# Optimization experiments

Measured on AMD Instinct MI355X. Metric: run time of the kernel, lower is better.

Reference implementation:

```python
import jax, jax.numpy as jnp
import numpy as np

EPS = 1e-5
K = 20

def knn_idx(x, k):
    # x: (B, C, N); returns indices of k nearest neighbors (incl. self), (B, N, k)
    xx = jnp.sum(x * x, axis=1, keepdims=True)            # (B,1,N)
    inner = -2.0 * jnp.einsum('bcn,bcm->bnm', x, x)       # (B,N,N)
    d = -jnp.swapaxes(xx, 1, 2) - inner - xx              # -||xi - xj||^2
    return jax.lax.top_k(d, k)[1]

def graph_feature(x, k):
    # x: (B, C, N) -> (B, 2C, N, k) with [neighbor - center, center]
    B, C, N = x.shape
    idx = knn_idx(x, k)                                   # (B,N,k)
    feat = jnp.swapaxes(x, 1, 2)                          # (B,N,C)
    nb = jax.vmap(lambda f, i: f[i])(feat, idx)           # (B,N,k,C) gather
    ctr = jnp.broadcast_to(feat[:, :, None, :], nb.shape)
    out = jnp.concatenate([nb - ctr, ctr], axis=-1)       # (B,N,k,2C)
    return jnp.transpose(out, (0, 3, 1, 2))

def bn(x, g, b, m, v):
    # inference-mode batchnorm over channel axis 1
    shape = (1, -1) + (1,) * (x.ndim - 2)
    inv = g / jnp.sqrt(v + EPS)
    return x * inv.reshape(shape) + (b - m * inv).reshape(shape)

def edge_block(x, W, g, b, m, v):
    f = graph_feature(x, K)                               # (B,2C,N,k)
    h = jnp.einsum('bcnk,oc->bonk', f, W)                 # 1x1 conv, no bias
    h = jax.nn.relu(bn(h, g, b, m, v))
    return jnp.max(h, axis=-1)                            # max over k -> (B,O,N)

def _forward(x, W1, W2, W3, W4, W5,
             g1, b1, m1, v1, g2, b2, m2, v2, g3, b3, m3, v3,
             g4, b4, m4, v4, g5, b5, m5, v5, g6, b6, m6, v6,
             g7, b7, m7, v7, L1W, L2W, L2b, L3W, L3b):
    x1 = edge_block(x, W1, g1, b1, m1, v1)                # (B,64,N)
    x2 = edge_block(x1, W2, g2, b2, m2, v2)               # (B,64,N)
    x3 = edge_block(x2, W3, g3, b3, m3, v3)               # (B,128,N)
    x4 = edge_block(x3, W4, g4, b4, m4, v4)               # (B,256,N)
    cat = jnp.concatenate([x1, x2, x3, x4], axis=1)       # (B,512,N)
    h = jnp.einsum('bcn,oc->bon', cat, W5)                # conv5 1x1
    h = jax.nn.relu(bn(h, g5, b5, m5, v5))
    h = jnp.max(h, axis=-1)                               # adaptive max pool -> (B,1024)
    h = jax.nn.relu(bn(h @ L1W.T, g6, b6, m6, v6))        # dropout = identity (eval)
    h = jax.nn.relu(bn(h @ L2W.T + L2b, g7, b7, m7, v7))
    return h @ L3W.T + L3b                                # (B, num_classes)

def _bn_params(keys, c):
    k0, k1, k2, k3 = keys
    g = jax.random.uniform(k0, (c,), jnp.float32, 0.5, 1.5)
    b = 0.1 * jax.random.normal(k1, (c,), jnp.float32)
    m = 0.1 * jax.random.normal(k2, (c,), jnp.float32)
    v = jax.random.uniform(k3, (c,), jnp.float32, 0.5, 1.5)
    return g, b, m, v

def setup_inputs() -> dict:
    key = jax.random.key(0)
    ks = jax.random.split(key, 40)
    d = {}
    d['x'] = jax.random.normal(ks[0], (8, 4, 1024), jnp.float32)
    def w(k, o, i):
        return jax.random.normal(k, (o, i), jnp.float32) * np.float32(np.sqrt(2.0 / i))
    d['W1'] = w(ks[1], 64, 8)
    d['W2'] = w(ks[2], 64, 128)
    d['W3'] = w(ks[3], 128, 128)
    d['W4'] = w(ks[4], 256, 256)
    d['W5'] = w(ks[5], 1024, 512)
    for i, c in enumerate([64, 64, 128, 256, 1024, 512, 256]):
        g, b, m, v = _bn_params(jax.random.split(ks[6 + i], 4), c)
        d[f'g{i+1}'], d[f'b{i+1}'], d[f'm{i+1}'], d[f'v{i+1}'] = g, b, m, v
    d['L1W'] = w(ks[20], 512, 1024)
    d['L2W'] = w(ks[21], 256, 512)
    d['L2b'] = 0.1 * jax.random.normal(ks[22], (256,), jnp.float32)
    d['L3W'] = w(ks[23], 8, 256)
    d['L3b'] = 0.1 * jax.random.normal(ks[24], (8,), jnp.float32)
    return d

def reference(x, W1, W2, W3, W4, W5,
              g1, b1, m1, v1, g2, b2, m2, v2, g3, b3, m3, v3,
              g4, b4, m4, v4, g5, b5, m5, v5, g6, b6, m6, v6,
              g7, b7, m7, v7, L1W, L2W, L2b, L3W, L3b):
    return _forward(x, W1, W2, W3, W4, W5,
                    g1, b1, m1, v1, g2, b2, m2, v2, g3, b3, m3, v3,
                    g4, b4, m4, v4, g5, b5, m5, v5, g6, b6, m6, v6,
                    g7, b7, m7, v7, L1W, L2W, L2b, L3W, L3b)
```

## Files before the change

### kernel.cpp

```cpp
#include <hip/hip_runtime.h>
#include <cstdint>

#define BB 8
#define NN 1024
#define KK 20
#define EPSV 1e-5f

typedef __attribute__((ext_vector_type(8))) short bf16x8;
typedef __attribute__((ext_vector_type(4))) float f32x4;

__device__ __forceinline__ unsigned fenc(float f) {
  unsigned u = __float_as_uint(f);
  return (u & 0x80000000u) ? ~u : (u | 0x80000000u);
}
__device__ __forceinline__ float fdec(unsigned u) {
  u = (u & 0x80000000u) ? (u & 0x7FFFFFFFu) : ~u;
  return __uint_as_float(u);
}
__device__ __forceinline__ unsigned short f2bf(float f) {
  unsigned u = __float_as_uint(f);
  unsigned r = u + 0x7FFFu + ((u >> 16) & 1u);
  return (unsigned short)(r >> 16);
}
__device__ __forceinline__ unsigned mbcnt64(unsigned long long m) {
  unsigned r = __builtin_amdgcn_mbcnt_lo((unsigned)m, 0u);
  return __builtin_amdgcn_mbcnt_hi((unsigned)(m >> 32), r);
}

template<int C>
__global__ __launch_bounds__(256) void xx_kernel(const float* __restrict__ x, float* __restrict__ xx) {
  int p = blockIdx.x * 256 + threadIdx.x;
  if (p >= BB * NN) return;
  int b = p >> 10, n = p & (NN - 1);
  const float* xb = x + (size_t)b * C * NN + n;
  float s = 0.f;
  #pragma unroll
  for (int c = 0; c < C; ++c) { float t = xb[(size_t)c * NN]; s = fmaf(t, t, s); }
  xx[p] = s;
}

template<int C>
__global__ __launch_bounds__(256) void dist_kernel(const float* __restrict__ x, const float* __restrict__ xx,
                                                   float* __restrict__ d, int b0) {
  constexpr int CC = (C < 32) ? C : 32;
  __shared__ __align__(16) float xi[CC][64];
  __shared__ __align__(16) float xj[CC][64];
  int bl = blockIdx.z, b = b0 + bl;
  int i0 = blockIdx.y * 64, j0 = blockIdx.x * 64;
  int t = threadIdx.x;
  int tj = t & 15, ti = t >> 4;
  float acc[4][4] = {};
  const float* xb = x + (size_t)b * C * NN;
  for (int c0 = 0; c0 < C; c0 += CC) {
    __syncthreads();
    for (int p = t; p < CC * 16; p += 256) {
      int cc = p >> 4, col = (p & 15) * 4;
      *reinterpret_cast<float4*>(&xi[cc][col]) =
        *reinterpret_cast<const float4*>(&xb[(size_t)(c0 + cc) * NN + i0 + col]);
      *reinterpret_cast<float4*>(&xj[cc][col]) =
        *reinterpret_cast<const float4*>(&xb[(size_t)(c0 + cc) * NN + j0 + col]);
    }
    __syncthreads();
    #pragma unroll
    for (int cc = 0; cc < CC; ++cc) {
      float4 A  = *reinterpret_cast<const float4*>(&xi[cc][ti * 4]);
      float4 Bv = *reinterpret_cast<const float4*>(&xj[cc][tj * 4]);
      float av[4] = {A.x, A.y, A.z, A.w};
      float bv[4] = {Bv.x, Bv.y, Bv.z, Bv.w};
      #pragma unroll
      for (int a = 0; a < 4; ++a)
        #pragma unroll
        for (int q = 0; q < 4; ++q)
          acc[a][q] = fmaf(av[a], bv[q], acc[a][q]);
    }
  }
  #pragma unroll
  for (int a = 0; a < 4; ++a) {
    int i = i0 + ti * 4 + a;
    float xxi = xx[b * NN + i];
    float4 o;
    o.x = 2.f * acc[a][0] - xxi - xx[b * NN + j0 + tj * 4 + 0];
    o.y = 2.f * acc[a][1] - xxi - xx[b * NN + j0 + tj * 4 + 1];
    o.z = 2.f * acc[a][2] - xxi - xx[b * NN + j0 + tj * 4 + 2];
    o.w = 2.f * acc[a][3] - xxi - xx[b * NN + j0 + tj * 4 + 3];
    *reinterpret_cast<float4*>(&d[((size_t)bl * NN + i) * NN + j0 + tj * 4]) = o;
  }
}

__global__ __launch_bounds__(256) void topk_kernel(const float* __restrict__ d, int* __restrict__ idx, int b0) {
  int t = threadIdx.x;
  int wave = t >> 6, lane = t & 63;
  int bl = blockIdx.y, b = b0 + bl;
  int i = blockIdx.x * 4 + wave;
  const float* row = d + ((size_t)bl * NN + i) * NN;

  unsigned v[16];
  #pragma unroll
  for (int p = 0; p < 4; ++p) {
    float4 f = *reinterpret_cast<const float4*>(&row[p * 256 + lane * 4]);
    v[p * 4 + 0] = fenc(f.x);
    v[p * 4 + 1] = fenc(f.y);
    v[p * 4 + 2] = fenc(f.z);
    v[p * 4 + 3] = fenc(f.w);
  }

  unsigned long long lo = 0, hi = 0xFFFFFFFFull;
  while (lo < hi) {
    unsigned long long mid = lo + ((hi - lo + 1) >> 1);
    unsigned mt = (unsigned)mid;
    int c = 0;
    #pragma unroll
    for (int e = 0; e < 16; ++e)
      c += __popcll(__ballot(v[e] >= mt));
    if (c >= KK) lo = mid; else hi = mid - 1;
  }
  unsigned T = (unsigned)lo;

  int* op = idx + ((size_t)b * NN + i) * KK;
  int base = 0, n1 = 0;
  #pragma unroll
  for (int e = 0; e < 16; ++e) {
    unsigned long long mask = __ballot(v[e] > T);
    unsigned mb = mbcnt64(mask);
    if (v[e] > T) op[base + mb] = (e >> 2) * 256 + lane * 4 + (e & 3);
    base += __popcll(mask);
  }
  n1 = base;
  int need = KK - n1;
  int neq = 0;
  #pragma unroll
  for (int e = 0; e < 16; ++e) neq += __popcll(__ballot(v[e] == T));
  if (neq == need) {
    #pragma unroll
    for (int e = 0; e < 16; ++e) {
      unsigned long long mask = __ballot(v[e] == T);
      unsigned mb = mbcnt64(mask);
      if (v[e] == T) op[base + mb] = (e >> 2) * 256 + lane * 4 + (e & 3);
      base += __popcll(mask);
    }
  } else {
    unsigned taken = 0;
    for (int s = 0; s < need; ++s) {
      int jm = 1 << 30;
      #pragma unroll
      for (int e = 0; e < 16; ++e) {
        if (v[e] == T && !((taken >> e) & 1u)) {
          int j = (e >> 2) * 256 + lane * 4 + (e & 3);
          jm = jm < j ? jm : j;
        }
      }
      #pragma unroll
      for (int st = 1; st < 64; st <<= 1) {
        int oj = __shfl_xor(jm, st);
        jm = jm < oj ? jm : oj;
      }
      if (lane == ((jm >> 2) & 63)) {
        int e = (((jm >> 8) << 2) | (jm & 3));
        taken |= 1u << e;
        op[base + s] = jm;
      }
    }
  }
}

template<int C, int O>
__global__ __launch_bounds__(256) void pgemm_kernel(const float* __restrict__ x, const float* __restrict__ W,
                                                    float* __restrict__ Plo, float* __restrict__ Phi) {
  constexpr int CC = (C < 64) ? C : 64;
  __shared__ __align__(16) float xs[CC][64];
  __shared__ __align__(16) float wls[CC][68];
  __shared__ __align__(16) float whs[CC][68];
  int b = blockIdx.z;
  int o0 = blockIdx.y * 64, n0 = blockIdx.x * 64;
  int t = threadIdx.x;
  int tn = t & 15, to = t >> 4;
  float accl[4][4] = {}, acch[4][4] = {};
  const float* xb = x + (size_t)b * C * NN;
  for (int c0 = 0; c0 < C; c0 += CC) {
    __syncthreads();
    for (int p = t; p < CC * 64; p += 256) {
      int cc = p >> 6, col = p & 63;
      xs[cc][col] = xb[(size_t)(c0 + cc) * NN + n0 + col];
    }
    for (int p = t; p < 64 * CC; p += 256) {
      int ol = p / CC, cc = p % CC;
      wls[cc][ol] = W[(size_t)(o0 + ol) * (2 * C) + c0 + cc];
      whs[cc][ol] = W[(size_t)(o0 + ol) * (2 * C) + C + c0 + cc];
    }
    __syncthreads();
    #pragma unroll
    for (int cc = 0; cc < CC; ++cc) {
      float4 X  = *reinterpret_cast<const float4*>(&xs[cc][tn * 4]);
      float4 Wl = *reinterpret_cast<const float4*>(&wls[cc][to * 4]);
      float4 Wh = *reinterpret_cast<const float4*>(&whs[cc][to * 4]);
      float xv[4] = {X.x, X.y, X.z, X.w};
      float wl[4] = {Wl.x, Wl.y, Wl.z, Wl.w};
      float wh[4] = {Wh.x, Wh.y, Wh.z, Wh.w};
      #pragma unroll
      for (int a = 0; a < 4; ++a)
        #pragma unroll
        for (int q = 0; q < 4; ++q) {
          accl[a][q] = fmaf(wl[a], xv[q], accl[a][q]);
          acch[a][q] = fmaf(wh[a], xv[q], acch[a][q]);
        }
    }
  }
  #pragma unroll
  for (int a = 0; a < 4; ++a) {
    int o = o0 + to * 4 + a;
    size_t base = ((size_t)b * O + o) * NN + n0 + tn * 4;
    float4 vl = {accl[a][0], accl[a][1], accl[a][2], accl[a][3]};
    float4 vh = {acch[a][0], acch[a][1], acch[a][2], acch[a][3]};
    *reinterpret_cast<float4*>(&Plo[base]) = vl;
    *reinterpret_cast<float4*>(&Phi[base]) = vh;
  }
}

__global__ __launch_bounds__(256) void edgemax_kernel(const float* __restrict__ Plo, const float* __restrict__ Phi,
    const int* __restrict__ idx, const float* __restrict__ g, const float* __restrict__ bt,
    const float* __restrict__ m, const float* __restrict__ v,
    float* __restrict__ xout, int O) {
  __shared__ __align__(16) float srow[4][NN];
  __shared__ __align__(16) float sphi[4][64];
  __shared__ int   sidx[64 * KK];
  __shared__ float sinv[32], ssb[32];
  int b = blockIdx.z, n0 = blockIdx.y * 64, o0 = blockIdx.x * 32;
  int t = threadIdx.x;
  if (t < 32) {
    float inv = g[o0 + t] / sqrtf(v[o0 + t] + EPSV);
    sinv[t] = inv; ssb[t] = bt[o0 + t] - m[o0 + t] * inv;
  }
  for (int p = t; p < 64 * KK; p += 256) sidx[p] = idx[((size_t)b * NN + n0) * KK + p];
  const float* plobase = Plo + (size_t)b * O * NN;
  const float* phibase = Phi + (size_t)b * O * NN;
  float4 cur0 = *reinterpret_cast<const float4*>(&plobase[(size_t)(o0 + 0) * NN + t * 4]);
  float4 cur1 = *reinterpret_cast<const float4*>(&plobase[(size_t)(o0 + 1) * NN + t * 4]);
  float4 cur2 = *reinterpret_cast<const float4*>(&plobase[(size_t)(o0 + 2) * NN + t * 4]);
  float4 cur3 = *reinterpret_cast<const float4*>(&plobase[(size_t)(o0 + 3) * NN + t * 4]);
  float4 curphi;
  if (t < 64) curphi = *reinterpret_cast<const float4*>(&phibase[(size_t)(o0 + (t >> 4)) * NN + n0 + (t & 15) * 4]);
  __syncthreads();
  int n = t >> 2, kg = t & 3;
  int j0 = sidx[n * KK + kg * 5 + 0];
  int j1 = sidx[n * KK + kg * 5 + 1];
  int j2 = sidx[n * KK + kg * 5 + 2];
  int j3 = sidx[n * KK + kg * 5 + 3];
  int j4 = sidx[n * KK + kg * 5 + 4];
  for (int oo = 0; oo < 32; oo += 4) {
    *reinterpret_cast<float4*>(&srow[0][t * 4]) = cur0;
    *reinterpret_cast<float4*>(&srow[1][t * 4]) = cur1;
    *reinterpret_cast<float4*>(&srow[2][t * 4]) = cur2;
    *reinterpret_cast<float4*>(&srow[3][t * 4]) = cur3;
    if (t < 64) *reinterpret_cast<float4*>(&sphi[t >> 4][(t & 15) * 4]) = curphi;
    if (oo < 28) {
      cur0 = *reinterpret_cast<const float4*>(&plobase[(size_t)(o0 + oo + 4) * NN + t * 4]);
      cur1 = *reinterpret_cast<const float4*>(&plobase[(size_t)(o0 + oo + 5) * NN + t * 4]);
      cur2 = *reinterpret_cast<const float4*>(&plobase[(size_t)(o0 + oo + 6) * NN + t * 4]);
      cur3 = *reinterpret_cast<const float4*>(&plobase[(size_t)(o0 + oo + 7) * NN + t * 4]);
      if (t < 64) curphi = *reinterpret_cast<const float4*>(&phibase[(size_t)(o0 + oo + 4 + (t >> 4)) * NN + n0 + (t & 15) * 4]);
    }
    __syncthreads();
    #pragma unroll
    for (int r = 0; r < 4; ++r) {
      float mx = srow[r][j0];
      mx = fmaxf(mx, srow[r][j1]);
      mx = fmaxf(mx, srow[r][j2]);
      mx = fmaxf(mx, srow[r][j3]);
      mx = fmaxf(mx, srow[r][j4]);
      mx = fmaxf(mx, __shfl_xor(mx, 1));
      mx = fmaxf(mx, __shfl_xor(mx, 2));
      if (kg == 0) {
        float z = mx - srow[r][n0 + n] + sphi[r][n];
        xout[((size_t)b * O + o0 + oo + r) * NN + n0 + n] =
          fmaxf(fmaf(z, sinv[oo + r], ssb[oo + r]), 0.f);
      }
    }
    __syncthreads();
  }
}

__global__ __launch_bounds__(256) void tcvt_kernel(const float* __restrict__ src,
    unsigned short* __restrict__ dst, int Csrc, int c0) {
  __shared__ float tile[64][65];
  int b = blockIdx.z, cb = blockIdx.y * 64, n0 = blockIdx.x * 64;
  int t = threadIdx.x;
  const float* s = src + ((size_t)b * Csrc + cb) * NN + n0;
  #pragma unroll
  for (int rr = 0; rr < 4; ++rr) {
    int r = (t >> 4) + rr * 16;
    float4 v = *reinterpret_cast<const float4*>(&s[(size_t)r * NN + (t & 15) * 4]);
    tile[r][(t & 15) * 4 + 0] = v.x;
    tile[r][(t & 15) * 4 + 1] = v.y;
    tile[r][(t & 15) * 4 + 2] = v.z;
    tile[r][(t & 15) * 4 + 3] = v.w;
  }
  __syncthreads();
  #pragma unroll
  for (int rr = 0; rr < 2; ++rr) {
    int chunk = t + 256 * rr;
    int n = chunk >> 3, cg = (chunk & 7) * 8;
    unsigned short u[8];
    #pragma unroll
    for (int j = 0; j < 8; ++j) u[j] = f2bf(tile[cg + j][n]);
    *reinterpret_cast<uint4*>(&dst[((size_t)b * NN + n0 + n) * 512 + c0 + cb + cg]) =
      *reinterpret_cast<const uint4*>(u);
  }
}

__global__ __launch_bounds__(256) void cvtw_kernel(const float* __restrict__ W, unsigned short* __restrict__ Wb) {
  int p = (blockIdx.x * 256 + threadIdx.x) * 4;
  float4 v = *reinterpret_cast<const float4*>(&W[p]);
  unsigned short u[4] = {f2bf(v.x), f2bf(v.y), f2bf(v.z), f2bf(v.w)};
  *reinterpret_cast<uint2*>(&Wb[p]) = *reinterpret_cast<const uint2*>(u);
}

__global__ __launch_bounds__(256) void pgemm4_mfma_kernel(const unsigned short* __restrict__ Xb,
    const unsigned short* __restrict__ W4b, float* __restrict__ Plo_t, float* __restrict__ Phi_t) {
  int b = blockIdx.z;
  int n0 = blockIdx.x * 128, o0 = blockIdx.y * 64;
  int t = threadIdx.x, lane = t & 63, w = t >> 6;
  int r = lane & 15, kc = lane >> 4;
  const unsigned short* A  = Xb + ((size_t)b * NN + n0 + w * 32 + r) * 512 + 128 + kc * 8;
  const unsigned short* Bw = W4b + ((size_t)(o0 + r)) * 256 + kc * 8;
  f32x4 accl0[4] = {}, accl1[4] = {}, acch0[4] = {}, acch1[4] = {};
  #pragma unroll
  for (int ks = 0; ks < 128; ks += 32) {
    bf16x8 a0 = *reinterpret_cast<const bf16x8*>(A + ks);
    bf16x8 a1 = *reinterpret_cast<const bf16x8*>(A + 16 * 512 + ks);
    #pragma unroll
    for (int j = 0; j < 4; ++j) {
      bf16x8 bl = *reinterpret_cast<const bf16x8*>(Bw + (size_t)j * 16 * 256 + ks);
      bf16x8 bh = *reinterpret_cast<const bf16x8*>(Bw + (size_t)j * 16 * 256 + 128 + ks);
      accl0[j] = __builtin_amdgcn_mfma_f32_16x16x32_bf16(a0, bl, accl0[j], 0, 0, 0);
      accl1[j] = __builtin_amdgcn_mfma_f32_16x16x32_bf16(a1, bl, accl1[j], 0, 0, 0);
      acch0[j] = __builtin_amdgcn_mfma_f32_16x16x32_bf16(a0, bh, acch0[j], 0, 0, 0);
      acch1[j] = __builtin_amdgcn_mfma_f32_16x16x32_bf16(a1, bh, acch1[j], 0, 0, 0);
    }
  }
  #pragma unroll
  for (int j = 0; j < 4; ++j) {
    #pragma unroll
    for (int reg = 0; reg < 4; ++reg) {
      size_t n_a = (size_t)b * NN + n0 + w * 32 + kc * 4 + reg;
      size_t n_b = n_a + 16;
      int oc = o0 + j * 16 + r;
      Plo_t[n_a * 256 + oc] = accl0[j][reg];
      Plo_t[n_b * 256 + oc] = accl1[j][reg];
      Phi_t[n_a * 256 + oc] = acch0[j][reg];
      Phi_t[n_b * 256 + oc] = acch1[j][reg];
    }
  }
}

__global__ __launch_bounds__(256) void edgemax4_kernel(const float* __restrict__ Plo_t,
    const float* __restrict__ Phi_t, const int* __restrict__ idx,
    const float* __restrict__ g, const float* __restrict__ bt,
    const float* __restrict__ m, const float* __restrict__ v,
    unsigned short* __restrict__ Xb) {
  int b = blockIdx.y, t = threadIdx.x;
  int n = blockIdx.x * 4 + (t >> 6);
  int oc = (t & 63) * 4;
  const int* ip = idx + ((size_t)b * NN + n) * KK;
  const float* base = Plo_t + (size_t)b * NN * 256;
  float4 mx = {-3.4e38f, -3.4e38f, -3.4e38f, -3.4e38f};
  #pragma unroll
  for (int k = 0; k < KK; ++k) {
    float4 vv = *reinterpret_cast<const float4*>(base + (size_t)ip[k] * 256 + oc);
    mx.x = fmaxf(mx.x, vv.x);
    mx.y = fmaxf(mx.y, vv.y);
    mx.z = fmaxf(mx.z, vv.z);
    mx.w = fmaxf(mx.w, vv.w);
  }
  float4 self = *reinterpret_cast<const float4*>(base + (size_t)n * 256 + oc);
  float4 ph = *reinterpret_cast<const float4*>(Phi_t + ((size_t)b * NN + n) * 256 + oc);
  float4 gg = *reinterpret_cast<const float4*>(g + oc);
  float4 bb = *reinterpret_cast<const float4*>(bt + oc);
  float4 mm = *reinterpret_cast<const float4*>(m + oc);
  float4 vv4 = *reinterpret_cast<const float4*>(v + oc);
  float mxa[4] = {mx.x, mx.y, mx.z, mx.w};
  float sfa[4] = {self.x, self.y, self.z, self.w};
  float pha[4] = {ph.x, ph.y, ph.z, ph.w};
  float ga[4] = {gg.x, gg.y, gg.z, gg.w};
  float ba[4] = {bb.x, bb.y, bb.z, bb.w};
  float ma[4] = {mm.x, mm.y, mm.z, mm.w};
  float va[4] = {vv4.x, vv4.y, vv4.z, vv4.w};
  unsigned short u[4];
  #pragma unroll
  for (int e = 0; e < 4; ++e) {
    float inv = ga[e] / sqrtf(va[e] + EPSV);
    float z = mxa[e] - sfa[e] + pha[e];
    float y = fmaxf(fmaf(z, inv, ba[e] - ma[e] * inv), 0.f);
    u[e] = f2bf(y);
  }
  *reinterpret_cast<uint2*>(&Xb[((size_t)b * NN + n) * 512 + 256 + oc]) =
    *reinterpret_cast<const uint2*>(u);
}

__global__ __launch_bounds__(256, 1) void conv5_mfma_kernel(const unsigned short* __restrict__ Xb,
    const unsigned short* __restrict__ W5b, unsigned* __restrict__ henc) {
  __shared__ __align__(16) unsigned short lA[4096 * 8];
  int b = blockIdx.z;
  int n0 = blockIdx.x * 128, o0 = blockIdx.y * 64;
  int t = threadIdx.x, lane = t & 63, w = t >> 6;
  int r = lane & 15, kc = lane >> 4;

  const unsigned short* B = Xb + ((size_t)b * NN + n0 + w * 32 + r) * 512 + kc * 8;
  bf16x8 b0[16], b1[16];
  #pragma unroll
  for (int ks = 0; ks < 16; ++ks) {
    b0[ks] = *reinterpret_cast<const bf16x8*>(B + ks * 32);
    b1[ks] = *reinterpret_cast<const bf16x8*>(B + 16 * 512 + ks * 32);
  }

  #pragma unroll
  for (int i = 0; i < 16; ++i) {
    int e = i * 256 + t;
    int le = e & 63, je = (e >> 6) & 3, kse = e >> 8;
    const unsigned short* src = W5b + ((size_t)(o0 + je * 16 + (le & 15))) * 512 + ((le >> 4) & 3) * 8 + kse * 32;
    *reinterpret_cast<uint4*>(&lA[(size_t)e * 8]) = *reinterpret_cast<const uint4*>(src);
  }
  __syncthreads();

  f32x4 acc00 = {}, acc01 = {}, acc10 = {}, acc11 = {};
  f32x4 acc20 = {}, acc21 = {}, acc30 = {}, acc31 = {};
  #pragma unroll
  for (int ks = 0; ks < 16; ++ks) {
    bf16x8 a0 = *reinterpret_cast<const bf16x8*>(&lA[(size_t)((ks * 4 + 0) * 64 + lane) * 8]);
    bf16x8 a1 = *reinterpret_cast<const bf16x8*>(&lA[(size_t)((ks * 4 + 1) * 64 + lane) * 8]);
    bf16x8 a2 = *reinterpret_cast<const bf16x8*>(&lA[(size_t)((ks * 4 + 2) * 64 + lane) * 8]);
    bf16x8 a3 = *reinterpret_cast<const bf16x8*>(&lA[(size_t)((ks * 4 + 3) * 64 + lane) * 8]);
    acc00 = __builtin_amdgcn_mfma_f32_16x16x32_bf16(a0, b0[ks], acc00, 0, 0, 0);
    acc01 = __builtin_amdgcn_mfma_f32_16x16x32_bf16(a0, b1[ks], acc01, 0, 0, 0);
    acc10 = __builtin_amdgcn_mfma_f32_16x16x32_bf16(a1, b0[ks], acc10, 0, 0, 0);
    acc11 = __builtin_amdgcn_mfma_f32_16x16x32_bf16(a1, b1[ks], acc11, 0, 0, 0);
    acc20 = __builtin_amdgcn_mfma_f32_16x16x32_bf16(a2, b0[ks], acc20, 0, 0, 0);
    acc21 = __builtin_amdgcn_mfma_f32_16x16x32_bf16(a2, b1[ks], acc21, 0, 0, 0);
    acc30 = __builtin_amdgcn_mfma_f32_16x16x32_bf16(a3, b0[ks], acc30, 0, 0, 0);
    acc31 = __builtin_amdgcn_mfma_f32_16x16x32_bf16(a3, b1[ks], acc31, 0, 0, 0);
  }

  f32x4 m0 = {fmaxf(acc00[0], acc01[0]), fmaxf(acc00[1], acc01[1]),
              fmaxf(acc00[2], acc01[2]), fmaxf(acc00[3], acc01[3])};
  f32x4 m1 = {fmaxf(acc10[0], acc11[0]), fmaxf(acc10[1], acc11[1]),
              fmaxf(acc10[2], acc11[2]), fmaxf(acc10[3], acc11[3])};
  f32x4 m2 = {fmaxf(acc20[0], acc21[0]), fmaxf(acc20[1], acc21[1]),
              fmaxf(acc20[2], acc21[2]), fmaxf(acc20[3], acc21[3])};
  f32x4 m3 = {fmaxf(acc30[0], acc31[0]), fmaxf(acc30[1], acc31[1]),
              fmaxf(acc30[2], acc31[2]), fmaxf(acc30[3], acc31[3])};
  #pragma unroll
  for (int st = 1; st < 16; st <<= 1) {
    #pragma unroll
    for (int reg = 0; reg < 4; ++reg) {
      m0[reg] = fmaxf(m0[reg], __shfl_xor(m0[reg], st));
      m1[reg] = fmaxf(m1[reg], __shfl_xor(m1[reg], st));
      m2[reg] = fmaxf(m2[reg], __shfl_xor(m2[reg], st));
      m3[reg] = fmaxf(m3[reg], __shfl_xor(m3[reg], st));
    }
  }
  if (r == 0) {
    #pragma unroll
    for (int reg = 0; reg < 4; ++reg) {
      atomicMax(&henc[b * 1024 + o0 + 0 * 16 + kc * 4 + reg], fenc(m0[reg]));
      atomicMax(&henc[b * 1024 + o0 + 1 * 16 + kc * 4 + reg], fenc(m1[reg]));
      atomicMax(&henc[b * 1024 + o0 + 2 * 16 + kc * 4 + reg], fenc(m2[reg]));
      atomicMax(&henc[b * 1024 + o0 + 3 * 16 + kc * 4 + reg], fenc(m3[reg]));
    }
  }
}

__global__ __launch_bounds__(256) void fc1_kernel(
    const unsigned* __restrict__ henc,
    const float* __restrict__ g5, const float* __restrict__ b5, const float* __restrict__ m5, const float* __restrict__ v5,
    const float* __restrict__ L1W,
    const float* __restrict__ g6, const float* __restrict__ b6, const float* __restrict__ m6, const float* __restrict__ v6,
    float* __restrict__ y1) {
  __shared__ float sh[1024];
  int b = blockIdx.y, t = threadIdx.x;
  int o0 = blockIdx.x * 64;
  for (int o = t; o < 1024; o += 256) {
    float f = fdec(henc[b * 1024 + o]);
    float inv = g5[o] / sqrtf(v5[o] + EPSV);
    sh[o] = fmaxf(fmaf(f, inv, b5[o] - m5[o] * inv), 0.f);
  }
  __syncthreads();
  int o = o0 + (t >> 2), part = t & 3;
  float acc = 0.f;
  const float4* w4 = reinterpret_cast<const float4*>(L1W + (size_t)o * 1024 + part * 256);
  const float4* h4 = reinterpret_cast<const float4*>(sh + part * 256);
  #pragma unroll 8
  for (int c = 0; c < 64; ++c) {
    float4 a = w4[c], q = h4[c];
    acc = fmaf(a.x, q.x, fmaf(a.y, q.y, fmaf(a.z, q.z, fmaf(a.w, q.w, acc))));
  }
  acc += __shfl_xor(acc, 1);
  acc += __shfl_xor(acc, 2);
  if (part == 0) {
    float inv = g6[o] / sqrtf(v6[o] + EPSV);
    y1[b * 512 + o] = fmaxf(fmaf(acc, inv, b6[o] - m6[o] * inv), 0.f);
  }
}

__global__ __launch_bounds__(256) void fc2_kernel(
    const float* __restrict__ y1,
    const float* __restrict__ L2W, const float* __restrict__ L2b,
    const float* __restrict__ g7, const float* __restrict__ b7, const float* __restrict__ m7, const float* __restrict__ v7,
    const float* __restrict__ L3W, const float* __restrict__ L3b,
    float* __restrict__ out) {
  __shared__ float sy1[512];
  __shared__ float sy2[256];
  int b = blockIdx.x, t = threadIdx.x;
  for (int o = t; o < 512; o += 256) sy1[o] = y1[b * 512 + o];
  __syncthreads();
  {
    int o = t;
    float acc = L2b[o];
    const float4* w4 = reinterpret_cast<const float4*>(L2W + (size_t)o * 512);
    const float4* q4 = reinterpret_cast<const float4*>(sy1);
    for (int c = 0; c < 128; ++c) {
      float4 a = w4[c], q = q4[c];
      acc = fmaf(a.x, q.x, fmaf(a.y, q.y, fmaf(a.z, q.z, fmaf(a.w, q.w, acc))));
    }
    float inv = g7[o] / sqrtf(v7[o] + EPSV);
    sy2[o] = fmaxf(fmaf(acc, inv, b7[o] - m7[o] * inv), 0.f);
  }
  __syncthreads();
  if (t < 8) {
    float acc = L3b[t];
    const float4* w4 = reinterpret_cast<const float4*>(L3W + (size_t)t * 256);
    const float4* q4 = reinterpret_cast<const float4*>(sy2);
    for (int c = 0; c < 64; ++c) {
      float4 a = w4[c], q = q4[c];
      acc = fmaf(a.x, q.x, fmaf(a.y, q.y, fmaf(a.z, q.z, fmaf(a.w, q.w, acc))));
    }
    out[b * 8 + t] = acc;
  }
}

extern "C" void kernel_launch(void* const* d_in, const int* in_sizes, int n_in,
                              void* d_out, int out_size, void* d_ws, size_t ws_size,
                              hipStream_t stream) {
  (void)in_sizes; (void)n_in; (void)out_size;
  const float* x   = (const float*)d_in[0];
  const float* W1  = (const float*)d_in[1];
  const float* W2  = (const float*)d_in[2];
  const float* W3  = (const float*)d_in[3];
  const float* W4  = (const float*)d_in[4];
  const float* W5  = (const float*)d_in[5];
  const float* bnp[7][4];
  for (int i = 0; i < 7; ++i)
    for (int j = 0; j < 4; ++j)
      bnp[i][j] = (const float*)d_in[6 + i * 4 + j];
  const float* L1W = (const float*)d_in[34];
  const float* L2W = (const float*)d_in[35];
  const float* L2b = (const float*)d_in[36];
  const float* L3W = (const float*)d_in[37];
  const float* L3b = (const float*)d_in[38];
  float* out = (float*)d_out;

  char* wsb = (char*)d_ws;
  size_t off = 0;
  auto alloc = [&](size_t bytes) -> void* {
    void* p = wsb + off; off += (bytes + 255) & ~(size_t)255; return p;
  };
  int*      idx  = (int*)     alloc((size_t)BB * NN * KK * 4);
  float*    xx   = (float*)   alloc((size_t)BB * NN * 4);
  float*    x1   = (float*)   alloc((size_t)BB * 64  * NN * 4);
  float*    x2   = (float*)   alloc((size_t)BB * 64  * NN * 4);
  float*    x3   = (float*)   alloc((size_t)BB * 128 * NN * 4);
  float*    Plo  = (float*)   alloc((size_t)BB * 256 * NN * 4);
  float*    Phi  = (float*)   alloc((size_t)BB * 256 * NN * 4);
  unsigned* henc = (unsigned*)alloc((size_t)BB * 1024 * 4);
  float*    y1   = (float*)   alloc((size_t)BB * 512 * 4);
  unsigned short* Xb  = (unsigned short*)alloc((size_t)BB * NN * 512 * 2);
  unsigned short* W5b = (unsigned short*)alloc((size_t)1024 * 512 * 2);
  unsigned short* W4b = (unsigned short*)alloc((size_t)256 * 256 * 2);
  size_t left = (ws_size > off) ? (ws_size - off) : 0;
  int nb = 8;
  while (nb > 1 && (size_t)nb * NN * NN * 4 > left) nb >>= 1;
  float* dbuf = (float*)(wsb + off);

  dim3 thr(256);
  #define KNN_PHASE(CIN, XIN)                                                              \
    xx_kernel<CIN><<<dim3(32), thr, 0, stream>>>(XIN, xx);                                 \
    for (int b0 = 0; b0 < BB; b0 += nb) {                                                  \
      dist_kernel<CIN><<<dim3(16, 16, nb), thr, 0, stream>>>(XIN, xx, dbuf, b0);           \
      topk_kernel<<<dim3(NN / 4, nb), thr, 0, stream>>>(dbuf, idx, b0);                    \
    }

  cvtw_kernel<<<dim3(512), thr, 0, stream>>>(W5, W5b);
  cvtw_kernel<<<dim3(64), thr, 0, stream>>>(W4, W4b);

  KNN_PHASE(4, x)
  pgemm_kernel<4, 64><<<dim3(16, 1, BB), thr, 0, stream>>>(x, W1, Plo, Phi);
  edgemax_kernel<<<dim3(2, 16, BB), thr, 0, stream>>>(Plo, Phi, idx,
      bnp[0][0], bnp[0][1], bnp[0][2], bnp[0][3], x1, 64);
  tcvt_kernel<<<dim3(16, 1, BB), thr, 0, stream>>>(x1, Xb, 64, 0);
  KNN_PHASE(64, x1)
  pgemm_kernel<64, 64><<<dim3(16, 1, BB), thr, 0, stream>>>(x1, W2, Plo, Phi);
  edgemax_kernel<<<dim3(2, 16, BB), thr, 0, stream>>>(Plo, Phi, idx,
      bnp[1][0], bnp[1][1], bnp[1][2], bnp[1][3], x2, 64);
  tcvt_kernel<<<dim3(16, 1, BB), thr, 0, stream>>>(x2, Xb, 64, 64);
  KNN_PHASE(64, x2)
  pgemm_kernel<64, 128><<<dim3(16, 2, BB), thr, 0, stream>>>(x2, W3, Plo, Phi);
  edgemax_kernel<<<dim3(4, 16, BB), thr, 0, stream>>>(Plo, Phi, idx,
      bnp[2][0], bnp[2][1], bnp[2][2], bnp[2][3], x3, 128);
  tcvt_kernel<<<dim3(16, 2, BB), thr, 0, stream>>>(x3, Xb, 128, 128);
  KNN_PHASE(128, x3)
  pgemm4_mfma_kernel<<<dim3(8, 4, BB), thr, 0, stream>>>(Xb, W4b, Plo, Phi);
  edgemax4_kernel<<<dim3(256, BB), thr, 0, stream>>>(Plo, Phi, idx,
      bnp[3][0], bnp[3][1], bnp[3][2], bnp[3][3], Xb);
  #undef KNN_PHASE

  hipMemsetAsync(henc, 0, (size_t)BB * 1024 * 4, stream);
  conv5_mfma_kernel<<<dim3(8, 16, BB), thr, 0, stream>>>(Xb, W5b, henc);

  fc1_kernel<<<dim3(8, BB), thr, 0, stream>>>(henc,
      bnp[4][0], bnp[4][1], bnp[4][2], bnp[4][3], L1W,
      bnp[5][0], bnp[5][1], bnp[5][2], bnp[5][3], y1);
  fc2_kernel<<<dim3(BB), thr, 0, stream>>>(y1,
      L2W, L2b, bnp[6][0], bnp[6][1], bnp[6][2], bnp[6][3], L3W, L3b, out);
}
```

Baseline: 416.5 us.

## Exploit distance matrix symmetry by computing only upper-triangle tiles

The pairwise distance kernel now launches only the 136 upper-triangular 64x64 tiles per batch instead of all 256. Each off-diagonal tile writes its result directly and also writes the transposed tile, staged through padded shared memory. This removes roughly half the dot-product FLOPs and input loads. The cost is extra shared-memory traffic and barriers, a small serial tile-index decode loop, and uneven work across blocks since diagonal tiles do less.

```diff
diff --git a/kernel.cpp b/kernel.cpp
--- a/kernel.cpp
+++ b/kernel.cpp
@@ -43,10 +43,16 @@
 __global__ __launch_bounds__(256) void dist_kernel(const float* __restrict__ x, const float* __restrict__ xx,
                                                    float* __restrict__ d, int b0) {
   constexpr int CC = (C < 32) ? C : 32;
-  __shared__ __align__(16) float xi[CC][64];
-  __shared__ __align__(16) float xj[CC][64];
+  constexpr int SM = (2 * CC * 64 > 64 * 65) ? 2 * CC * 64 : 64 * 65;
+  __shared__ __align__(16) float smem[SM];
+  float* xi = smem;
+  float* xj = smem + CC * 64;
   int bl = blockIdx.z, b = b0 + bl;
-  int i0 = blockIdx.y * 64, j0 = blockIdx.x * 64;
+  int qq0 = blockIdx.x;
+  int by = 0;
+  while (qq0 >= 16 - by) { qq0 -= 16 - by; ++by; }
+  int bx = by + qq0;
+  int i0 = by * 64, j0 = bx * 64;
   int t = threadIdx.x;
   int tj = t & 15, ti = t >> 4;
   float acc[4][4] = {};
@@ -55,16 +61,16 @@
     __syncthreads();
     for (int p = t; p < CC * 16; p += 256) {
       int cc = p >> 4, col = (p & 15) * 4;
-      *reinterpret_cast<float4*>(&xi[cc][col]) =
+      *reinterpret_cast<float4*>(&xi[cc * 64 + col]) =
         *reinterpret_cast<const float4*>(&xb[(size_t)(c0 + cc) * NN + i0 + col]);
-      *reinterpret_cast<float4*>(&xj[cc][col]) =
+      *reinterpret_cast<float4*>(&xj[cc * 64 + col]) =
         *reinterpret_cast<const float4*>(&xb[(size_t)(c0 + cc) * NN + j0 + col]);
     }
     __syncthreads();
     #pragma unroll
     for (int cc = 0; cc < CC; ++cc) {
-      float4 A  = *reinterpret_cast<const float4*>(&xi[cc][ti * 4]);
-      float4 Bv = *reinterpret_cast<const float4*>(&xj[cc][tj * 4]);
+      float4 A  = *reinterpret_cast<const float4*>(&xi[cc * 64 + ti * 4]);
+      float4 Bv = *reinterpret_cast<const float4*>(&xj[cc * 64 + tj * 4]);
       float av[4] = {A.x, A.y, A.z, A.w};
       float bv[4] = {Bv.x, Bv.y, Bv.z, Bv.w};
       #pragma unroll
@@ -84,6 +90,26 @@
     o.z = 2.f * acc[a][2] - xxi - xx[b * NN + j0 + tj * 4 + 2];
     o.w = 2.f * acc[a][3] - xxi - xx[b * NN + j0 + tj * 4 + 3];
     *reinterpret_cast<float4*>(&d[((size_t)bl * NN + i) * NN + j0 + tj * 4]) = o;
+  }
+  if (by != bx) {
+    __syncthreads();
+    #pragma unroll
+    for (int a = 0; a < 4; ++a)
+      #pragma unroll
+      for (int q = 0; q < 4; ++q)
+        smem[(ti * 4 + a) * 65 + tj * 4 + q] = acc[a][q];
+    __syncthreads();
+    #pragma unroll
+    for (int a = 0; a < 4; ++a) {
+      int jr = j0 + ti * 4 + a;
+      float xxr = xx[b * NN + jr];
+      float4 o;
+      o.x = 2.f * smem[(tj * 4 + 0) * 65 + ti * 4 + a] - xxr - xx[b * NN + i0 + tj * 4 + 0];
+      o.y = 2.f * smem[(tj * 4 + 1) * 65 + ti * 4 + a] - xxr - xx[b * NN + i0 + tj * 4 + 1];
+      o.z = 2.f * smem[(tj * 4 + 2) * 65 + ti * 4 + a] - xxr - xx[b * NN + i0 + tj * 4 + 2];
+      o.w = 2.f * smem[(tj * 4 + 3) * 65 + ti * 4 + a] - xxr - xx[b * NN + i0 + tj * 4 + 3];
+      *reinterpret_cast<float4*>(&d[((size_t)bl * NN + jr) * NN + i0 + tj * 4]) = o;
+    }
   }
 }
 
@@ -583,7 +609,7 @@
   #define KNN_PHASE(CIN, XIN)                                                              \
     xx_kernel<CIN><<<dim3(32), thr, 0, stream>>>(XIN, xx);                                 \
     for (int b0 = 0; b0 < BB; b0 += nb) {                                                  \
-      dist_kernel<CIN><<<dim3(16, 16, nb), thr, 0, stream>>>(XIN, xx, dbuf, b0);           \
+      dist_kernel<CIN><<<dim3(136, 1, nb), thr, 0, stream>>>(XIN, xx, dbuf, b0);           \
       topk_kernel<<<dim3(NN / 4, nb), thr, 0, stream>>>(dbuf, idx, b0);                    \
     }
 
```

Result: faster. 402.1 us (-3.5%).
